# Optimization experiments

Measured on AMD Instinct MI355X. Metric: run time of the kernel, lower is better.

## Reference

```python
import jax, jax.numpy as jnp
import numpy as np

DIM, N_HEADS, N_KV, HEAD_DIM = 5120, 40, 8, 128
MAX_BS, MAX_SEQ = 8, 4096
BSZ, SEQLEN, START_POS = 8, 1, 4095


def setup_inputs() -> dict:
    key = jax.random.key(0)
    ks = jax.random.split(key, 12)
    x = jax.random.normal(ks[0], (BSZ, SEQLEN, DIM), jnp.float32)
    # RoPE angles for positions [START_POS, START_POS+SEQLEN)
    inv_freq = 1.0 / (10000.0 ** (np.arange(0, HEAD_DIM, 2, dtype=np.float32) / HEAD_DIM))
    t = np.arange(START_POS, START_POS + SEQLEN, dtype=np.float32)
    ang = np.outer(t, inv_freq)  # [seqlen, head_dim//2]
    freqs_cis = jnp.asarray(np.stack([np.cos(ang), np.sin(ang)], axis=-1), jnp.float32)
    cache_k = jax.random.normal(ks[1], (MAX_BS, MAX_SEQ, N_KV, HEAD_DIM), jnp.float32)
    cache_v = jax.random.normal(ks[2], (MAX_BS, MAX_SEQ, N_KV, HEAD_DIM), jnp.float32)
    s = 0.02
    wq = jax.random.normal(ks[3], (DIM, N_HEADS * HEAD_DIM), jnp.float32) * s
    bq = jax.random.normal(ks[4], (N_HEADS * HEAD_DIM,), jnp.float32) * s
    wk = jax.random.normal(ks[5], (DIM, N_KV * HEAD_DIM), jnp.float32) * s
    bk = jax.random.normal(ks[6], (N_KV * HEAD_DIM,), jnp.float32) * s
    wv = jax.random.normal(ks[7], (DIM, N_KV * HEAD_DIM), jnp.float32) * s
    bv = jax.random.normal(ks[8], (N_KV * HEAD_DIM,), jnp.float32) * s
    wo = jax.random.normal(ks[9], (N_HEADS * HEAD_DIM, DIM), jnp.float32) * s
    bo = jax.random.normal(ks[10], (DIM,), jnp.float32) * s
    return dict(x=x, start_pos=START_POS, freqs_cis=freqs_cis, cache_k=cache_k,
                cache_v=cache_v, wq=wq, bq=bq, wk=wk, bk=bk, wv=wv, bv=bv, wo=wo, bo=bo)


def _apply_rope(xq, xk, freqs_cis):
    # x*: [b, s, h, hd]; freqs_cis: [s, hd//2, 2] (cos, sin)
    cos = freqs_cis[None, :, None, :, 0]
    sin = freqs_cis[None, :, None, :, 1]
    def rot(x):
        xr = x.reshape(*x.shape[:-1], HEAD_DIM // 2, 2)
        xe, xo = xr[..., 0], xr[..., 1]
        out = jnp.stack([xe * cos - xo * sin, xe * sin + xo * cos], axis=-1)
        return out.reshape(x.shape)
    return rot(xq), rot(xk)


def reference(x, start_pos, freqs_cis, cache_k, cache_v, wq, bq, wk, bk, wv, bv, wo, bo):
    bsz, seqlen, _ = x.shape
    n_rep = N_HEADS // N_KV
    xq = (x @ wq + bq).reshape(bsz, seqlen, N_HEADS, HEAD_DIM)
    xk = (x @ wk + bk).reshape(bsz, seqlen, N_KV, HEAD_DIM)
    xv = (x @ wv + bv).reshape(bsz, seqlen, N_KV, HEAD_DIM)
    xq, xk = _apply_rope(xq, xk, freqs_cis)
    # KV-cache scatter (in-place write in the original)
    cache_k = jax.lax.dynamic_update_slice(cache_k, xk, (0, start_pos, 0, 0))
    cache_v = jax.lax.dynamic_update_slice(cache_v, xv, (0, start_pos, 0, 0))
    klen = start_pos + seqlen
    keys = cache_k[:bsz, :klen]    # [b, t, n_kv, hd]
    values = cache_v[:bsz, :klen]
    # GQA attention without materializing the repeat_kv expansion (same math)
    qg = xq.reshape(bsz, seqlen, N_KV, n_rep, HEAD_DIM)
    scale = 1.0 / np.sqrt(HEAD_DIM)
    scores = jnp.einsum('bsgrd,btgd->bgrst', qg, keys) * scale  # [b,g,r,s,t]
    probs = jax.nn.softmax(scores.astype(jnp.float32), axis=-1).astype(x.dtype)
    out = jnp.einsum('bgrst,btgd->bsgrd', probs, values)
    out = out.reshape(bsz, seqlen, N_HEADS * HEAD_DIM)
    return out @ wo + bo
```

## Files before the change

### kernel.cpp

```cpp
#include <hip/hip_runtime.h>
#include <hip/hip_bf16.h>
#include <math.h>

#define DIM   5120
#define NH    40
#define NKV   8
#define HD    128
#define BS    8
#define KLEN  4096
#define NEWT  4095
#define NREP  5

#define ODQKV 7168
#define NKC   32
#define KCH   (DIM / NKC)

#define NCHUNK 32
#define CH_T   (KLEN / NCHUNK)
#define WAVE_T (CH_T / 4)
#define NPART  NCHUNK

#define WS_Q       0
#define WS_K       (WS_Q + BS * DIM)
#define WS_V       (WS_K + BS * NKV * HD)
#define WS_ATTN    (WS_V + BS * NKV * HD)
#define WS_SCRATCH (WS_ATTN + BS * DIM)

__global__ __launch_bounds__(256) void qkv_partial_k(
    const float* __restrict__ x, const float* __restrict__ wq,
    const float* __restrict__ wk, const float* __restrict__ wv,
    float* __restrict__ part) {
  const int cb = blockIdx.x % 14;
  const int kc = blockIdx.x / 14;
  const int c0 = cb * 512 + threadIdx.x * 2;

  const float* w; int OD, j;
  if (c0 < 5120)      { w = wq; OD = 5120; j = c0; }
  else if (c0 < 6144) { w = wk; OD = 1024; j = c0 - 5120; }
  else                { w = wv; OD = 1024; j = c0 - 6144; }

  const int i0 = kc * KCH;
  float ax[BS], ay[BS];
#pragma unroll
  for (int b = 0; b < BS; ++b) { ax[b] = 0.f; ay[b] = 0.f; }

  const float* wp = w + (size_t)i0 * OD + j;
  const float* xp = x + i0;
#pragma unroll 4
  for (int ii = 0; ii < KCH; ++ii) {
    const float2 wv2 = *(const float2*)&wp[(size_t)ii * OD];
#pragma unroll
    for (int b = 0; b < BS; ++b) {
      const float xb = xp[b * DIM + ii];
      ax[b] = fmaf(xb, wv2.x, ax[b]);
      ay[b] = fmaf(xb, wv2.y, ay[b]);
    }
  }
#pragma unroll
  for (int b = 0; b < BS; ++b)
    *(float2*)&part[((size_t)kc * BS + b) * ODQKV + c0] = make_float2(ax[b], ay[b]);
}

__global__ __launch_bounds__(256) void qkv_reduce_k(
    const float* __restrict__ part, const float* __restrict__ bq,
    const float* __restrict__ bk, const float* __restrict__ bv,
    const float* __restrict__ fc, float* __restrict__ qws,
    float* __restrict__ kws, float* __restrict__ vws) {
  int g = blockIdx.x * 256 + threadIdx.x;
  if (g >= BS * (ODQKV / 2)) return;
  int b  = g / (ODQKV / 2);
  int cp = g - b * (ODQKV / 2);
  int c0 = cp * 2;

  float sx = 0.f, sy = 0.f;
  for (int kc = 0; kc < NKC; ++kc) {
    const float2 p = *(const float2*)&part[((size_t)kc * BS + b) * ODQKV + c0];
    sx += p.x; sy += p.y;
  }

  const float scale = 0.088388347648318447f;
  if (c0 < 5120) {
    sx += bq[c0]; sy += bq[c0 + 1];
    int jf = (c0 & 127) >> 1;
    float cs = fc[2 * jf], sn = fc[2 * jf + 1];
    qws[b * DIM + c0]     = (sx * cs - sy * sn) * scale;
    qws[b * DIM + c0 + 1] = (sx * sn + sy * cs) * scale;
  } else if (c0 < 6144) {
    int jj = c0 - 5120;
    sx += bk[jj]; sy += bk[jj + 1];
    int jf = (jj & 127) >> 1;
    float cs = fc[2 * jf], sn = fc[2 * jf + 1];
    kws[b * NKV * HD + jj]     = sx * cs - sy * sn;
    kws[b * NKV * HD + jj + 1] = sx * sn + sy * cs;
  } else {
    int jj = c0 - 6144;
    vws[b * NKV * HD + jj]     = sx + bv[jj];
    vws[b * NKV * HD + jj + 1] = sy + bv[jj + 1];
  }
}

__global__ __launch_bounds__(256) void attn_partial_k(
    const float* __restrict__ ck, const float* __restrict__ cv,
    const float* __restrict__ qws, const float* __restrict__ kws,
    const float* __restrict__ vws, float* __restrict__ pM,
    float* __restrict__ pL, float* __restrict__ pO) {
  const int blk   = blockIdx.x;
  const int chunk = blk & (NCHUNK - 1);
  const int bh    = blk / NCHUNK;
  const int h     = bh & (NKV - 1);
  const int b     = bh / NKV;
  const int wave  = threadIdx.x >> 6;
  const int lane  = threadIdx.x & 63;
  const int grp   = lane >> 4;
  const int sl    = lane & 15;
  const int t0    = chunk * CH_T + wave * WAVE_T;

  float4 qa[NREP], qb[NREP];
#pragma unroll
  for (int r = 0; r < NREP; ++r) {
    const float* qp = &qws[b * DIM + (h * NREP + r) * HD + 8 * sl];
    qa[r] = *(const float4*)qp;
    qb[r] = *(const float4*)(qp + 4);
  }

  float m[NREP], l[NREP], o[NREP][8];
#pragma unroll
  for (int r = 0; r < NREP; ++r) {
    m[r] = -1e30f; l[r] = 0.f;
#pragma unroll
    for (int j = 0; j < 8; ++j) o[r][j] = 0.f;
  }

  const float* kbase = &ck[((size_t)b * KLEN * NKV + h) * HD];
  const float* vbase = &cv[((size_t)b * KLEN * NKV + h) * HD];

  auto step = [&](const float4 ka, const float4 kb,
                  const float4 va, const float4 vb) {
    float s[NREP];
#pragma unroll
    for (int r = 0; r < NREP; ++r) {
      s[r] = qa[r].x * ka.x + qa[r].y * ka.y + qa[r].z * ka.z + qa[r].w * ka.w
           + qb[r].x * kb.x + qb[r].y * kb.y + qb[r].z * kb.z + qb[r].w * kb.w;
    }
#pragma unroll
    for (int off = 1; off < 16; off <<= 1) {
#pragma unroll
      for (int r = 0; r < NREP; ++r) s[r] += __shfl_xor(s[r], off, 64);
    }
    const float vv[8] = {va.x, va.y, va.z, va.w, vb.x, vb.y, vb.z, vb.w};
#pragma unroll
    for (int r = 0; r < NREP; ++r) {
      if (s[r] <= m[r]) {
        float p = __expf(s[r] - m[r]);
        l[r] += p;
#pragma unroll
        for (int j = 0; j < 8; ++j) o[r][j] = fmaf(p, vv[j], o[r][j]);
      } else {
        float rs = __expf(m[r] - s[r]);
        l[r] = fmaf(l[r], rs, 1.f);
#pragma unroll
        for (int j = 0; j < 8; ++j) o[r][j] = fmaf(o[r][j], rs, vv[j]);
        m[r] = s[r];
      }
    }
  };

  int niter = WAVE_T / 4;
  const bool tail = (t0 + WAVE_T - 1 == NEWT);
  if (tail) --niter;

  const float* kp = kbase + (size_t)(t0 + grp) * (NKV * HD) + 8 * sl;
  const float* vp = vbase + (size_t)(t0 + grp) * (NKV * HD) + 8 * sl;
#pragma unroll 2
  for (int i = 0; i < niter; ++i) {
    const float4 ka = *(const float4*)kp;
    const float4 kb = *(const float4*)(kp + 4);
    const float4 va = *(const float4*)vp;
    const float4 vb = *(const float4*)(vp + 4);
    kp += 4 * NKV * HD;
    vp += 4 * NKV * HD;
    step(ka, kb, va, vb);
  }
  if (tail) {
    const int t = t0 + WAVE_T - 4 + grp;
    const float* kr = (t == NEWT) ? &kws[(b * NKV + h) * HD]
                                  : kbase + (size_t)t * (NKV * HD);
    const float* vr = (t == NEWT) ? &vws[(b * NKV + h) * HD]
                                  : vbase + (size_t)t * (NKV * HD);
    const float4 ka = *(const float4*)(kr + 8 * sl);
    const float4 kb = *(const float4*)(kr + 8 * sl + 4);
    const float4 va = *(const float4*)(vr + 8 * sl);
    const float4 vb = *(const float4*)(vr + 8 * sl + 4);
    step(ka, kb, va, vb);
  }

#pragma unroll
  for (int off = 16; off <= 32; off <<= 1) {
#pragma unroll
    for (int r = 0; r < NREP; ++r) {
      float mo = __shfl_xor(m[r], off, 64);
      float lo = __shfl_xor(l[r], off, 64);
      float oo[8];
#pragma unroll
      for (int j = 0; j < 8; ++j) oo[j] = __shfl_xor(o[r][j], off, 64);
      float mn = fmaxf(m[r], mo);
      float ea = __expf(m[r] - mn);
      float eb = __expf(mo - mn);
      l[r] = l[r] * ea + lo * eb;
#pragma unroll
      for (int j = 0; j < 8; ++j) o[r][j] = o[r][j] * ea + oo[j] * eb;
      m[r] = mn;
    }
  }

  __shared__ float smO[4][NREP][HD];
  __shared__ float smM[4][NREP], smL[4][NREP];
  if (grp == 0) {
#pragma unroll
    for (int r = 0; r < NREP; ++r) {
      float* sp = &smO[wave][r][8 * sl];
      *(float4*)sp       = make_float4(o[r][0], o[r][1], o[r][2], o[r][3]);
      *(float4*)(sp + 4) = make_float4(o[r][4], o[r][5], o[r][6], o[r][7]);
    }
    if (sl == 0) {
#pragma unroll
      for (int r = 0; r < NREP; ++r) { smM[wave][r] = m[r]; smL[wave][r] = l[r]; }
    }
  }
  __syncthreads();

  const int tid = threadIdx.x;
  if (tid < HD) {
    const int d  = tid;
    const int pb = bh * NCHUNK + chunk;
#pragma unroll
    for (int r = 0; r < NREP; ++r) {
      float M = fmaxf(fmaxf(smM[0][r], smM[1][r]), fmaxf(smM[2][r], smM[3][r]));
      float acc = 0.f, lsum = 0.f;
#pragma unroll
      for (int w = 0; w < 4; ++w) {
        float e = __expf(smM[w][r] - M);
        acc  = fmaf(e, smO[w][r][d], acc);
        lsum = fmaf(e, smL[w][r], lsum);
      }
      pO[((size_t)pb * NREP + r) * HD + d] = acc;
      if (d == 0) { pM[pb * NREP + r] = M; pL[pb * NREP + r] = lsum; }
    }
  }
}

__global__ __launch_bounds__(256) void attn_combine_k(
    const float* __restrict__ pM, const float* __restrict__ pL,
    const float* __restrict__ pO, float* __restrict__ attn) {
  const int bh  = blockIdx.x;
  const int h   = bh & (NKV - 1);
  const int b   = bh / NKV;
  const int tid = threadIdx.x;
  __shared__ float ml[NREP * NPART], ll[NREP * NPART];
  __shared__ float wgt[NREP * NPART];
  __shared__ float Linv[NREP];

  for (int idx = tid; idx < NREP * NPART; idx += 256) {
    int r = idx / NPART, w = idx - r * NPART;
    ml[idx] = pM[(bh * NPART + w) * NREP + r];
    ll[idx] = pL[(bh * NPART + w) * NREP + r];
  }
  __syncthreads();
  for (int idx = tid; idx < NREP * NPART; idx += 256) {
    int r = idx / NPART;
    float M = -1e30f;
    for (int w = 0; w < NPART; ++w) M = fmaxf(M, ml[r * NPART + w]);
    float e = __expf(ml[idx] - M);
    wgt[idx] = e;
    ll[idx] *= e;
  }
  __syncthreads();
  if (tid < NREP) {
    float L = 0.f;
    for (int w = 0; w < NPART; ++w) L += ll[tid * NPART + w];
    Linv[tid] = 1.f / L;
  }
  __syncthreads();

  for (int oidx = tid; oidx < NREP * HD; oidx += 256) {
    int r = oidx >> 7, d = oidx & 127;
    float acc = 0.f;
    for (int w = 0; w < NPART; ++w)
      acc += wgt[r * NPART + w] * pO[((size_t)(bh * NPART + w) * NREP + r) * HD + d];
    attn[b * DIM + (h * NREP + r) * HD + d] = acc * Linv[r];
  }
}

__global__ __launch_bounds__(256) void out_partial_k(
    const float* __restrict__ attn, const float* __restrict__ wo,
    float* __restrict__ part) {
  const int cb = blockIdx.x % 10;
  const int kc = blockIdx.x / 10;
  const int c0 = cb * 512 + threadIdx.x * 2;

  const int i0 = kc * KCH;
  float ax[BS], ay[BS];
#pragma unroll
  for (int b = 0; b < BS; ++b) { ax[b] = 0.f; ay[b] = 0.f; }

  const float* wp = wo + (size_t)i0 * DIM + c0;
  const float* xp = attn + i0;
#pragma unroll 4
  for (int ii = 0; ii < KCH; ++ii) {
    const float2 wv2 = *(const float2*)&wp[(size_t)ii * DIM];
#pragma unroll
    for (int b = 0; b < BS; ++b) {
      const float xb = xp[b * DIM + ii];
      ax[b] = fmaf(xb, wv2.x, ax[b]);
      ay[b] = fmaf(xb, wv2.y, ay[b]);
    }
  }
#pragma unroll
  for (int b = 0; b < BS; ++b)
    *(float2*)&part[((size_t)kc * BS + b) * DIM + c0] = make_float2(ax[b], ay[b]);
}

__global__ __launch_bounds__(256) void out_reduce_k(
    const float* __restrict__ part, const float* __restrict__ bo,
    float* __restrict__ out) {
  int g = blockIdx.x * 256 + threadIdx.x;
  if (g >= BS * DIM) return;
  int b = g / DIM, c = g - b * DIM;
  float s = 0.f;
  for (int kc = 0; kc < NKC; ++kc) s += part[((size_t)kc * BS + b) * DIM + c];
  out[g] = s + bo[c];
}

extern "C" void kernel_launch(void* const* d_in, const int* in_sizes, int n_in,
                              void* d_out, int out_size, void* d_ws, size_t ws_size,
                              hipStream_t stream) {
  const float* x  = (const float*)d_in[0];
  const float* fc = (const float*)d_in[2];
  const float* ck = (const float*)d_in[3];
  const float* cv = (const float*)d_in[4];
  const float* wq = (const float*)d_in[5];
  const float* bq = (const float*)d_in[6];
  const float* wk = (const float*)d_in[7];
  const float* bk = (const float*)d_in[8];
  const float* wv = (const float*)d_in[9];
  const float* bv = (const float*)d_in[10];
  const float* wo = (const float*)d_in[11];
  const float* bo = (const float*)d_in[12];

  float* ws      = (float*)d_ws;
  float* qws     = ws + WS_Q;
  float* kws     = ws + WS_K;
  float* vws     = ws + WS_V;
  float* attn    = ws + WS_ATTN;
  float* scratch = ws + WS_SCRATCH;

  qkv_partial_k<<<14 * NKC, 256, 0, stream>>>(x, wq, wk, wv, scratch);
  qkv_reduce_k<<<(BS * (ODQKV / 2) + 255) / 256, 256, 0, stream>>>(
      scratch, bq, bk, bv, fc, qws, kws, vws);

  float* pM = scratch;
  float* pL = pM + 64 * NPART * NREP;
  float* pO = pL + 64 * NPART * NREP;
  attn_partial_k<<<64 * NCHUNK, 256, 0, stream>>>(ck, cv, qws, kws, vws, pM, pL, pO);
  attn_combine_k<<<64, 256, 0, stream>>>(pM, pL, pO, attn);

  out_partial_k<<<10 * NKC, 256, 0, stream>>>(attn, wo, scratch);
  out_reduce_k<<<(BS * DIM + 255) / 256, 256, 0, stream>>>(scratch, bo, (float*)d_out);
}
```

Before: 139.5 us.

## Replace online softmax with two-pass block softmax via LDS scores in attention partial kernel

The attention partial kernel now computes all QK scores for its chunk first and stores them in shared memory. It then runs a block-wide max and exp-sum reduction and does a separate PV accumulation pass. This removes the per-token branchy online-softmax rescaling and the per-wave max/sum merge, leaving plain FMAs in the V loop. The costs are extra barriers and LDS traffic, and K and V loads are no longer overlapped in the same loop, which may reduce memory-level parallelism.

```diff
diff --git a/kernel.cpp b/kernel.cpp
--- a/kernel.cpp
+++ b/kernel.cpp
@@ -109,11 +109,17 @@
   const int bh    = blk / NCHUNK;
   const int h     = bh & (NKV - 1);
   const int b     = bh / NKV;
-  const int wave  = threadIdx.x >> 6;
-  const int lane  = threadIdx.x & 63;
+  const int tid   = threadIdx.x;
+  const int wave  = tid >> 6;
+  const int lane  = tid & 63;
   const int grp   = lane >> 4;
   const int sl    = lane & 15;
   const int t0    = chunk * CH_T + wave * WAVE_T;
+
+  __shared__ float s_lds[CH_T * NREP];
+  __shared__ float red[NREP * 8];
+  __shared__ float Msh[NREP], Lsh[NREP];
+  __shared__ float smO[4][NREP][HD];
 
   float4 qa[NREP], qb[NREP];
 #pragma unroll
@@ -123,98 +129,139 @@
     qb[r] = *(const float4*)(qp + 4);
   }
 
-  float m[NREP], l[NREP], o[NREP][8];
-#pragma unroll
-  for (int r = 0; r < NREP; ++r) {
-    m[r] = -1e30f; l[r] = 0.f;
-#pragma unroll
-    for (int j = 0; j < 8; ++j) o[r][j] = 0.f;
-  }
-
   const float* kbase = &ck[((size_t)b * KLEN * NKV + h) * HD];
   const float* vbase = &cv[((size_t)b * KLEN * NKV + h) * HD];
 
-  auto step = [&](const float4 ka, const float4 kb,
-                  const float4 va, const float4 vb) {
-    float s[NREP];
-#pragma unroll
-    for (int r = 0; r < NREP; ++r) {
-      s[r] = qa[r].x * ka.x + qa[r].y * ka.y + qa[r].z * ka.z + qa[r].w * ka.w
-           + qb[r].x * kb.x + qb[r].y * kb.y + qb[r].z * kb.z + qb[r].w * kb.w;
-    }
-#pragma unroll
-    for (int off = 1; off < 16; off <<= 1) {
-#pragma unroll
-      for (int r = 0; r < NREP; ++r) s[r] += __shfl_xor(s[r], off, 64);
-    }
-    const float vv[8] = {va.x, va.y, va.z, va.w, vb.x, vb.y, vb.z, vb.w};
-#pragma unroll
-    for (int r = 0; r < NREP; ++r) {
-      if (s[r] <= m[r]) {
-        float p = __expf(s[r] - m[r]);
-        l[r] += p;
-#pragma unroll
-        for (int j = 0; j < 8; ++j) o[r][j] = fmaf(p, vv[j], o[r][j]);
-      } else {
-        float rs = __expf(m[r] - s[r]);
-        l[r] = fmaf(l[r], rs, 1.f);
-#pragma unroll
-        for (int j = 0; j < 8; ++j) o[r][j] = fmaf(o[r][j], rs, vv[j]);
-        m[r] = s[r];
+  int niter = WAVE_T / 4;
+  const bool tailw = (t0 + WAVE_T == KLEN);
+  if (tailw) --niter;
+
+  {
+    const float* kp = kbase + (size_t)(t0 + grp) * (NKV * HD) + 8 * sl;
+#pragma unroll 4
+    for (int i = 0; i < niter; ++i) {
+      const float4 ka = *(const float4*)kp;
+      const float4 kb = *(const float4*)(kp + 4);
+      kp += 4 * NKV * HD;
+      float s[NREP];
+#pragma unroll
+      for (int r = 0; r < NREP; ++r) {
+        s[r] = qa[r].x * ka.x + qa[r].y * ka.y + qa[r].z * ka.z + qa[r].w * ka.w
+             + qb[r].x * kb.x + qb[r].y * kb.y + qb[r].z * kb.z + qb[r].w * kb.w;
       }
-    }
-  };
-
-  int niter = WAVE_T / 4;
-  const bool tail = (t0 + WAVE_T - 1 == NEWT);
-  if (tail) --niter;
-
-  const float* kp = kbase + (size_t)(t0 + grp) * (NKV * HD) + 8 * sl;
-  const float* vp = vbase + (size_t)(t0 + grp) * (NKV * HD) + 8 * sl;
-#pragma unroll 2
-  for (int i = 0; i < niter; ++i) {
-    const float4 ka = *(const float4*)kp;
-    const float4 kb = *(const float4*)(kp + 4);
-    const float4 va = *(const float4*)vp;
-    const float4 vb = *(const float4*)(vp + 4);
-    kp += 4 * NKV * HD;
-    vp += 4 * NKV * HD;
-    step(ka, kb, va, vb);
-  }
-  if (tail) {
-    const int t = t0 + WAVE_T - 4 + grp;
-    const float* kr = (t == NEWT) ? &kws[(b * NKV + h) * HD]
-                                  : kbase + (size_t)t * (NKV * HD);
-    const float* vr = (t == NEWT) ? &vws[(b * NKV + h) * HD]
-                                  : vbase + (size_t)t * (NKV * HD);
-    const float4 ka = *(const float4*)(kr + 8 * sl);
-    const float4 kb = *(const float4*)(kr + 8 * sl + 4);
-    const float4 va = *(const float4*)(vr + 8 * sl);
-    const float4 vb = *(const float4*)(vr + 8 * sl + 4);
-    step(ka, kb, va, vb);
+#pragma unroll
+      for (int off = 1; off < 16; off <<= 1) {
+#pragma unroll
+        for (int r = 0; r < NREP; ++r) s[r] += __shfl_xor(s[r], off, 64);
+      }
+      const int tl = wave * WAVE_T + 4 * i + grp;
+      float sv = (sl == 0) ? s[0] : (sl == 1) ? s[1] : (sl == 2) ? s[2]
+               : (sl == 3) ? s[3] : s[4];
+      if (sl < NREP) s_lds[tl * NREP + sl] = sv;
+    }
+    if (tailw) {
+      const int t  = t0 + WAVE_T - 4 + grp;
+      const float* kr = (t == NEWT) ? &kws[(b * NKV + h) * HD]
+                                    : kbase + (size_t)t * (NKV * HD);
+      const float4 ka = *(const float4*)(kr + 8 * sl);
+      const float4 kb = *(const float4*)(kr + 8 * sl + 4);
+      float s[NREP];
+#pragma unroll
+      for (int r = 0; r < NREP; ++r) {
+        s[r] = qa[r].x * ka.x + qa[r].y * ka.y + qa[r].z * ka.z + qa[r].w * ka.w
+             + qb[r].x * kb.x + qb[r].y * kb.y + qb[r].z * kb.z + qb[r].w * kb.w;
+      }
+#pragma unroll
+      for (int off = 1; off < 16; off <<= 1) {
+#pragma unroll
+        for (int r = 0; r < NREP; ++r) s[r] += __shfl_xor(s[r], off, 64);
+      }
+      const int tl = wave * WAVE_T + WAVE_T - 4 + grp;
+      float sv = (sl == 0) ? s[0] : (sl == 1) ? s[1] : (sl == 2) ? s[2]
+               : (sl == 3) ? s[3] : s[4];
+      if (sl < NREP) s_lds[tl * NREP + sl] = sv;
+    }
+  }
+  __syncthreads();
+
+  if (tid < NREP * 8) {
+    const int r = tid >> 3, seg = tid & 7;
+    float mx = -1e30f;
+    for (int k = 0; k < 16; ++k) mx = fmaxf(mx, s_lds[(seg * 16 + k) * NREP + r]);
+    red[tid] = mx;
+  }
+  __syncthreads();
+  if (tid < NREP) {
+    float mx = red[tid * 8];
+    for (int k = 1; k < 8; ++k) mx = fmaxf(mx, red[tid * 8 + k]);
+    Msh[tid] = mx;
+  }
+  __syncthreads();
+  for (int idx = tid; idx < CH_T * NREP; idx += 256)
+    s_lds[idx] = __expf(s_lds[idx] - Msh[idx % NREP]);
+  __syncthreads();
+  if (tid < NREP * 8) {
+    const int r = tid >> 3, seg = tid & 7;
+    float sm = 0.f;
+    for (int k = 0; k < 16; ++k) sm += s_lds[(seg * 16 + k) * NREP + r];
+    red[tid] = sm;
+  }
+  __syncthreads();
+  if (tid < NREP) {
+    float L = 0.f;
+    for (int k = 0; k < 8; ++k) L += red[tid * 8 + k];
+    Lsh[tid] = L;
+  }
+
+  float o[NREP][8];
+#pragma unroll
+  for (int r = 0; r < NREP; ++r)
+#pragma unroll
+    for (int j = 0; j < 8; ++j) o[r][j] = 0.f;
+
+  {
+    const float* vp = vbase + (size_t)(t0 + grp) * (NKV * HD) + 8 * sl;
+#pragma unroll 4
+    for (int i = 0; i < niter; ++i) {
+      const float4 va = *(const float4*)vp;
+      const float4 vb = *(const float4*)(vp + 4);
+      vp += 4 * NKV * HD;
+      const int tl = wave * WAVE_T + 4 * i + grp;
+      float p[NREP];
+#pragma unroll
+      for (int r = 0; r < NREP; ++r) p[r] = s_lds[tl * NREP + r];
+      const float vv[8] = {va.x, va.y, va.z, va.w, vb.x, vb.y, vb.z, vb.w};
+#pragma unroll
+      for (int r = 0; r < NREP; ++r)
+#pragma unroll
+        for (int j = 0; j < 8; ++j) o[r][j] = fmaf(p[r], vv[j], o[r][j]);
+    }
+    if (tailw) {
+      const int t  = t0 + WAVE_T - 4 + grp;
+      const float* vr = (t == NEWT) ? &vws[(b * NKV + h) * HD]
+                                    : vbase + (size_t)t * (NKV * HD);
+      const float4 va = *(const float4*)(vr + 8 * sl);
+      const float4 vb = *(const float4*)(vr + 8 * sl + 4);
+      const int tl = wave * WAVE_T + WAVE_T - 4 + grp;
+      float p[NREP];
+#pragma unroll
+      for (int r = 0; r < NREP; ++r) p[r] = s_lds[tl * NREP + r];
+      const float vv[8] = {va.x, va.y, va.z, va.w, vb.x, vb.y, vb.z, vb.w};
+#pragma unroll
+      for (int r = 0; r < NREP; ++r)
+#pragma unroll
+        for (int j = 0; j < 8; ++j) o[r][j] = fmaf(p[r], vv[j], o[r][j]);
+    }
   }
 
 #pragma unroll
   for (int off = 16; off <= 32; off <<= 1) {
 #pragma unroll
-    for (int r = 0; r < NREP; ++r) {
-      float mo = __shfl_xor(m[r], off, 64);
-      float lo = __shfl_xor(l[r], off, 64);
-      float oo[8];
-#pragma unroll
-      for (int j = 0; j < 8; ++j) oo[j] = __shfl_xor(o[r][j], off, 64);
-      float mn = fmaxf(m[r], mo);
-      float ea = __expf(m[r] - mn);
-      float eb = __expf(mo - mn);
-      l[r] = l[r] * ea + lo * eb;
-#pragma unroll
-      for (int j = 0; j < 8; ++j) o[r][j] = o[r][j] * ea + oo[j] * eb;
-      m[r] = mn;
-    }
-  }
-
-  __shared__ float smO[4][NREP][HD];
-  __shared__ float smM[4][NREP], smL[4][NREP];
+    for (int r = 0; r < NREP; ++r)
+#pragma unroll
+      for (int j = 0; j < 8; ++j) o[r][j] += __shfl_xor(o[r][j], off, 64);
+  }
+
   if (grp == 0) {
 #pragma unroll
     for (int r = 0; r < NREP; ++r) {
@@ -222,29 +269,17 @@
       *(float4*)sp       = make_float4(o[r][0], o[r][1], o[r][2], o[r][3]);
       *(float4*)(sp + 4) = make_float4(o[r][4], o[r][5], o[r][6], o[r][7]);
     }
-    if (sl == 0) {
-#pragma unroll
-      for (int r = 0; r < NREP; ++r) { smM[wave][r] = m[r]; smL[wave][r] = l[r]; }
-    }
-  }
-  __syncthreads();
-
-  const int tid = threadIdx.x;
+  }
+  __syncthreads();
+
   if (tid < HD) {
     const int d  = tid;
     const int pb = bh * NCHUNK + chunk;
 #pragma unroll
     for (int r = 0; r < NREP; ++r) {
-      float M = fmaxf(fmaxf(smM[0][r], smM[1][r]), fmaxf(smM[2][r], smM[3][r]));
-      float acc = 0.f, lsum = 0.f;
-#pragma unroll
-      for (int w = 0; w < 4; ++w) {
-        float e = __expf(smM[w][r] - M);
-        acc  = fmaf(e, smO[w][r][d], acc);
-        lsum = fmaf(e, smL[w][r], lsum);
-      }
+      float acc = smO[0][r][d] + smO[1][r][d] + smO[2][r][d] + smO[3][r][d];
       pO[((size_t)pb * NREP + r) * HD + d] = acc;
-      if (d == 0) { pM[pb * NREP + r] = M; pL[pb * NREP + r] = lsum; }
+      if (d == 0) { pM[pb * NREP + r] = Msh[r]; pL[pb * NREP + r] = Lsh[r]; }
     }
   }
 }
```

After: 130.9 us. 1.07x faster.
